# Performance work log

Hardware: AMD Instinct MI355X
Metric: run time of the kernel (lower is better)

The kernel has to match this reference:

```python
import jax, jax.numpy as jnp
import numpy as np

DIM = 512; DEPTH = 2; HEADS = 8; DIM_HEAD = 64; INNER = HEADS * DIM_HEAD
MEM = 16; TOPK = 8; FF = 4 * DIM
NUM_BUCKETS = 32; MAX_DIST = 128
EPS = 1e-5


def _layernorm(x, g, b):
    m = jnp.mean(x, axis=-1, keepdims=True)
    v = jnp.var(x, axis=-1, keepdims=True)
    return (x - m) * jax.lax.rsqrt(v + EPS) * g + b


def _rel_bucket(rel_pos):
    # T5 relative-position bucketing, causal=True (as hardcoded in Encoder)
    num_buckets = NUM_BUCKETS // 2  # 16
    n = -rel_pos
    ret = (n < 0).astype(jnp.int32) * num_buckets
    n = jnp.abs(n)
    max_exact = num_buckets // 2  # 8
    is_small = n < max_exact
    nf = jnp.maximum(n, 1).astype(jnp.float32)  # safe log; masked by is_small where n==0
    val_if_large = max_exact + (
        jnp.log(nf / max_exact) / np.log(MAX_DIST / max_exact) * (num_buckets - max_exact)
    ).astype(jnp.int32)
    val_if_large = jnp.minimum(val_if_large, num_buckets - 1)
    return ret + jnp.where(is_small, n, val_if_large)


def setup_inputs() -> dict:
    key = jax.random.key(0)
    ks = jax.random.split(key, 16)
    B, N = 2, 2048
    w = lambda k, shape, s=0.02: jax.random.normal(k, shape, jnp.float32) * s
    return {
        "x": jax.random.normal(ks[0], (B, N, DIM), jnp.float32),
        "ln1_g": jnp.ones((DEPTH, DIM), jnp.float32),
        "ln1_b": jnp.zeros((DEPTH, DIM), jnp.float32),
        "Wq": w(ks[1], (DEPTH, DIM, INNER)),
        "Wkv": w(ks[2], (DEPTH, DIM, 2 * INNER)),
        "Wo": w(ks[3], (DEPTH, INNER, DIM)),
        "bo": jnp.zeros((DEPTH, DIM), jnp.float32),
        "pre_proj": w(ks[4], (DEPTH, HEADS, HEADS), 1.0),  # torch.randn init
        "mem_k": w(ks[5], (DEPTH, HEADS, MEM, DIM_HEAD), 1.0),
        "mem_v": w(ks[6], (DEPTH, HEADS, MEM, DIM_HEAD), 1.0),
        "ln2_g": jnp.ones((DEPTH, DIM), jnp.float32),
        "ln2_b": jnp.zeros((DEPTH, DIM), jnp.float32),
        "W1": w(ks[7], (DEPTH, DIM, FF)),
        "b1": jnp.zeros((DEPTH, FF), jnp.float32),
        "W2": w(ks[8], (DEPTH, FF, DIM)),
        "b2": jnp.zeros((DEPTH, DIM), jnp.float32),
        "rel_emb": w(ks[9], (NUM_BUCKETS, HEADS)),
    }


def reference(x, ln1_g, ln1_b, Wq, Wkv, Wo, bo, pre_proj, mem_k, mem_v,
              ln2_g, ln2_b, W1, b1, W2, b2, rel_emb):
    B, N, _ = x.shape
    J = N + MEM  # keys include num_mem_kv memory slots
    scale = DIM_HEAD ** -0.5
    # relative position bias, shape (1, H, N, J); same for every layer
    rel = jnp.arange(J)[None, :] - jnp.arange(N)[:, None]
    bias = jnp.transpose(rel_emb[_rel_bucket(rel)], (2, 0, 1))[None]

    for l in range(DEPTH):
        # --- PreNorm(Attention) + residual ---
        h = _layernorm(x, ln1_g[l], ln1_b[l])
        q = (h @ Wq[l]).reshape(B, N, HEADS, DIM_HEAD).transpose(0, 2, 1, 3)
        k, v = jnp.split(h @ Wkv[l], 2, axis=-1)
        k = k.reshape(B, N, HEADS, DIM_HEAD).transpose(0, 2, 1, 3)
        v = v.reshape(B, N, HEADS, DIM_HEAD).transpose(0, 2, 1, 3)
        k = jnp.concatenate([jnp.broadcast_to(mem_k[l], (B, HEADS, MEM, DIM_HEAD)), k], axis=2)
        v = jnp.concatenate([jnp.broadcast_to(mem_v[l], (B, HEADS, MEM, DIM_HEAD)), v], axis=2)
        dots = jnp.einsum('bhid,bhjd->bhij', q, k) * scale
        dots = jnp.einsum('bhij,hk->bkij', dots, pre_proj[l])  # talking heads (pre-softmax)
        dots = dots + bias
        # sparse top-k masking: keep only values >= k-th largest per row
        thr = jax.lax.top_k(dots, TOPK)[0][..., -1:]
        dots = jnp.where(dots < thr, -jnp.inf, dots)
        attn = jax.nn.softmax(dots, axis=-1)
        out = jnp.einsum('bhij,bhjd->bhid', attn, v)
        out = out.transpose(0, 2, 1, 3).reshape(B, N, INNER)
        x = out @ Wo[l] + bo[l] + x
        # --- PreNorm(FeedForward) + residual ---
        h2 = _layernorm(x, ln2_g[l], ln2_b[l])
        x = jax.nn.gelu(h2 @ W1[l] + b1[l], approximate=False) @ W2[l] + b2[l] + x
    return x
```

## Files before the change

### kernel.cpp

```cpp
#include <hip/hip_runtime.h>
#include <cmath>

typedef __bf16 bf16;
typedef __attribute__((ext_vector_type(8))) __bf16 bf16x8;
typedef __attribute__((ext_vector_type(4))) __bf16 bf16x4;
typedef __attribute__((ext_vector_type(4))) float f32x4;

#define NB 2
#define NSEQ 2048
#define NDIM 512
#define NHEADS 8
#define DHEAD 64
#define NMEM 16
#define NJ 2064
#define NJP 2176
#define NFF 2048
#define NROWS (NB*NSEQ)

enum { EPI_QKV = 0, EPI_GELUSPLIT = 1, EPI_RESID = 2 };

template<int BM, int BN, int WAVES_M, int WAVES_N, int EPI>
__global__ __launch_bounds__(256)
void gemm_split(const bf16* __restrict__ A, const bf16* __restrict__ B,
                void* __restrict__ Cv, const float* __restrict__ bias,
                void* __restrict__ Cv2,
                int K, int lda, int ldb, int ldc, int loA, int loB)
{
  constexpr int BK = 32;
  constexpr int WM = BM / WAVES_M;
  constexpr int WN = BN / WAVES_N;
  constexpr int MF = WM / 16;
  constexpr int NF = WN / 16;
  constexpr int AI = (BM * BK * 2) / 4096;
  constexpr int BI = (BN * BK * 2) / 4096;
  __shared__ bf16 Ash[2][BM * BK];
  __shared__ bf16 Asl[2][BM * BK];
  __shared__ bf16 Bsh[2][BN * BK];
  __shared__ bf16 Bsl[2][BN * BK];

  const int bm0 = blockIdx.x * BM;
  const int bn0 = blockIdx.y * BN;
  const int t = threadIdx.x;
  const int wave = t >> 6, lane = t & 63;
  const int wr = wave / WAVES_N, wc = wave % WAVES_N;
  const int sr = t >> 2, sc = t & 3;
  const int frow = lane & 15, fk = (lane >> 4) * 8;

  auto stage = [&](int buf, int k0) {
#pragma unroll
    for (int qi = 0; qi < AI; ++qi) {
      const long long ro = (long long)(bm0 + qi * 64 + sr) * lda + (k0 + sc * 8);
      __builtin_amdgcn_global_load_lds(
          (const __attribute__((address_space(1))) void*)(A + ro),
          (__attribute__((address_space(3))) void*)(&Ash[buf][qi * 2048 + wave * 512]), 16, 0, 0);
      __builtin_amdgcn_global_load_lds(
          (const __attribute__((address_space(1))) void*)(A + ro + loA),
          (__attribute__((address_space(3))) void*)(&Asl[buf][qi * 2048 + wave * 512]), 16, 0, 0);
    }
#pragma unroll
    for (int qi = 0; qi < BI; ++qi) {
      const long long ro = (long long)(bn0 + qi * 64 + sr) * ldb + (k0 + sc * 8);
      __builtin_amdgcn_global_load_lds(
          (const __attribute__((address_space(1))) void*)(B + ro),
          (__attribute__((address_space(3))) void*)(&Bsh[buf][qi * 2048 + wave * 512]), 16, 0, 0);
      __builtin_amdgcn_global_load_lds(
          (const __attribute__((address_space(1))) void*)(B + ro + loB),
          (__attribute__((address_space(3))) void*)(&Bsl[buf][qi * 2048 + wave * 512]), 16, 0, 0);
    }
  };

  f32x4 acc[MF][NF] = {};

  stage(0, 0);
  __syncthreads();
  int cur = 0;
  for (int k0 = 0; k0 < K; k0 += BK) {
    if (k0 + BK < K) stage(cur ^ 1, k0 + BK);
    bf16x8 afh[MF], afl[MF], bfh[NF], bfl[NF];
#pragma unroll
    for (int m = 0; m < MF; m++) {
      afh[m] = *(const bf16x8*)(&Ash[cur][(wr * WM + m * 16 + frow) * BK + fk]);
      afl[m] = *(const bf16x8*)(&Asl[cur][(wr * WM + m * 16 + frow) * BK + fk]);
    }
#pragma unroll
    for (int n = 0; n < NF; n++) {
      bfh[n] = *(const bf16x8*)(&Bsh[cur][(wc * WN + n * 16 + frow) * BK + fk]);
      bfl[n] = *(const bf16x8*)(&Bsl[cur][(wc * WN + n * 16 + frow) * BK + fk]);
    }
#pragma unroll
    for (int m = 0; m < MF; m++)
#pragma unroll
      for (int n = 0; n < NF; n++) {
        acc[m][n] = __builtin_amdgcn_mfma_f32_16x16x32_bf16(afh[m], bfh[n], acc[m][n], 0, 0, 0);
        acc[m][n] = __builtin_amdgcn_mfma_f32_16x16x32_bf16(afl[m], bfh[n], acc[m][n], 0, 0, 0);
        acc[m][n] = __builtin_amdgcn_mfma_f32_16x16x32_bf16(afh[m], bfl[n], acc[m][n], 0, 0, 0);
      }
    __syncthreads();
    cur ^= 1;
  }

#pragma unroll
  for (int m = 0; m < MF; m++) {
#pragma unroll
    for (int n = 0; n < NF; n++) {
      const int row0 = bm0 + wr * WM + m * 16 + (lane >> 4) * 4;
      const int col = bn0 + wc * WN + n * 16 + (lane & 15);
#pragma unroll
      for (int r = 0; r < 4; r++) {
        const float v = acc[m][n][r];
        const long long i = row0 + r;
        if (EPI == EPI_QKV) {
          if (col < NDIM) {
            const float vq = v * 0.125f;
            bf16* base = (bf16*)Cv;
            const long long ih = i * (long long)(2 * NDIM) + col;
            bf16 h = (bf16)vq;
            base[ih] = h;
            base[ih + NDIM] = (bf16)(vq - (float)h);
          } else {
            ((float*)Cv2)[i * (long long)(2 * NDIM) + (col - NDIM)] = v;
          }
        } else if (EPI == EPI_GELUSPLIT) {
          float u = v + bias[col];
          float gl = 0.5f * u * (1.0f + erff(u * 0.7071067811865476f));
          const long long ih = i * (long long)(2 * ldc) + col;
          bf16 h = (bf16)gl;
          ((bf16*)Cv)[ih] = h;
          ((bf16*)Cv)[ih + ldc] = (bf16)(gl - (float)h);
        } else {
          float* xp = ((float*)Cv) + i * ldc + col;
          *xp = *xp + v + bias[col];
        }
      }
    }
  }
}

__global__ __launch_bounds__(256)
void s_gemm_direct(const bf16* __restrict__ Qs, const bf16* __restrict__ Ks,
                   float* __restrict__ S)
{
  const int h = blockIdx.z;
  const int bm0 = blockIdx.x * 128;
  const int bn0 = blockIdx.y * 128;
  const int t = threadIdx.x;
  const int wave = t >> 6, lane = t & 63;
  const int wr = wave >> 1, wc = wave & 1;
  const int frow = lane & 15, fk = (lane >> 4) * 8;

  bf16x8 ah[4][2], al[4][2];
#pragma unroll
  for (int m = 0; m < 4; m++)
#pragma unroll
    for (int kk = 0; kk < 2; kk++) {
      const bf16* ap = Qs + (long long)(bm0 + wr * 64 + m * 16 + frow) * 1024
                     + h * 64 + kk * 32 + fk;
      ah[m][kk] = *(const bf16x8*)(ap);
      al[m][kk] = *(const bf16x8*)(ap + 512);
    }

  f32x4 acc[4][4] = {};
#pragma unroll
  for (int n = 0; n < 4; n++) {
    bf16x8 bh[2], bl[2];
#pragma unroll
    for (int kk = 0; kk < 2; kk++) {
      const bf16* bp = Ks + (long long)(bn0 + wc * 64 + n * 16 + frow) * 1024
                     + h * 64 + kk * 32 + fk;
      bh[kk] = *(const bf16x8*)(bp);
      bl[kk] = *(const bf16x8*)(bp + 512);
    }
#pragma unroll
    for (int m = 0; m < 4; m++)
#pragma unroll
      for (int kk = 0; kk < 2; kk++) {
        acc[m][n] = __builtin_amdgcn_mfma_f32_16x16x32_bf16(ah[m][kk], bh[kk], acc[m][n], 0, 0, 0);
        acc[m][n] = __builtin_amdgcn_mfma_f32_16x16x32_bf16(al[m][kk], bh[kk], acc[m][n], 0, 0, 0);
        acc[m][n] = __builtin_amdgcn_mfma_f32_16x16x32_bf16(ah[m][kk], bl[kk], acc[m][n], 0, 0, 0);
      }
  }

#pragma unroll
  for (int m = 0; m < 4; m++) {
#pragma unroll
    for (int n = 0; n < 4; n++) {
      const int row0 = bm0 + wr * 64 + m * 16 + (lane >> 4) * 4;
      const int col = bn0 + wc * 64 + n * 16 + (lane & 15);
#pragma unroll
      for (int r = 0; r < 4; r++)
        S[(long long)(row0 + r) * (NHEADS * NJP) + h * NJP + col] = acc[m][n][r];
    }
  }
}

__global__ __launch_bounds__(256)
void ln_kernel(const float* __restrict__ x, const float* __restrict__ g,
               const float* __restrict__ b, bf16* __restrict__ out)
{
  const int row = blockIdx.x * 4 + (threadIdx.x >> 6);
  const int lane = threadIdx.x & 63;
  const float* xr = x + (long long)row * NDIM;
  float4 a0 = ((const float4*)xr)[lane];
  float4 a1 = ((const float4*)xr)[lane + 64];
  float s = a0.x + a0.y + a0.z + a0.w + a1.x + a1.y + a1.z + a1.w;
  float ss = a0.x * a0.x + a0.y * a0.y + a0.z * a0.z + a0.w * a0.w
           + a1.x * a1.x + a1.y * a1.y + a1.z * a1.z + a1.w * a1.w;
#pragma unroll
  for (int d = 1; d < 64; d <<= 1) {
    s += __shfl_xor(s, d, 64);
    ss += __shfl_xor(ss, d, 64);
  }
  const float mean = s * (1.0f / NDIM);
  const float var = ss * (1.0f / NDIM) - mean * mean;
  const float rs = rsqrtf(var + 1e-5f);
  float4 g0 = ((const float4*)g)[lane], g1 = ((const float4*)g)[lane + 64];
  float4 b0 = ((const float4*)b)[lane], b1 = ((const float4*)b)[lane + 64];
  bf16* orow = out + (long long)row * (2 * NDIM);
  float y[8] = {
    (a0.x - mean) * rs * g0.x + b0.x, (a0.y - mean) * rs * g0.y + b0.y,
    (a0.z - mean) * rs * g0.z + b0.z, (a0.w - mean) * rs * g0.w + b0.w,
    (a1.x - mean) * rs * g1.x + b1.x, (a1.y - mean) * rs * g1.y + b1.y,
    (a1.z - mean) * rs * g1.z + b1.z, (a1.w - mean) * rs * g1.w + b1.w };
  bf16x4 h0, h1, l0, l1;
#pragma unroll
  for (int j = 0; j < 4; j++) {
    bf16 h = (bf16)y[j];      h0[j] = h;  l0[j] = (bf16)(y[j] - (float)h);
    bf16 h2 = (bf16)y[4 + j]; h1[j] = h2; l1[j] = (bf16)(y[4 + j] - (float)h2);
  }
  *(bf16x4*)(orow + lane * 4) = h0;
  *(bf16x4*)(orow + 256 + lane * 4) = h1;
  *(bf16x4*)(orow + 512 + lane * 4) = l0;
  *(bf16x4*)(orow + 768 + lane * 4) = l1;
}

__global__ __launch_bounds__(256)
void build_ks(const float* __restrict__ kv, const float* __restrict__ mem_k_l,
              bf16* __restrict__ Ks)
{
  const long long idx = (long long)blockIdx.x * 256 + threadIdx.x;
  const int c = (int)(idx & 511);
  const int j = (int)((idx >> 9) % NJP);
  const int bb = (int)(idx / ((long long)NJP * NDIM));
  const int h = c >> 6, d = c & 63;
  float kval;
  if (j < NMEM) kval = mem_k_l[(h * NMEM + j) * DHEAD + d];
  else if (j < NJ) kval = kv[(long long)(bb * NSEQ + (j - NMEM)) * (2 * NDIM) + c];
  else kval = 0.f;
  bf16 hv = (bf16)kval;
  const long long ro = ((long long)bb * NJP + j) * (2 * NDIM) + c;
  Ks[ro] = hv;
  Ks[ro + NDIM] = (bf16)(kval - (float)hv);
}

__global__ __launch_bounds__(512)
void mix_topk_gather(const float* __restrict__ S, const float* __restrict__ kv,
                     const float* __restrict__ mem_v_l, const float* __restrict__ pp,
                     const float* __restrict__ table, bf16* __restrict__ obufs,
                     int b)
{
  __shared__ float sm[4 * NJP];
  const int i = blockIdx.x;
  const int k = threadIdx.x >> 6;
  const int lane = threadIdx.x & 63;
  const float* srow = S + (long long)i * (NHEADS * NJP);

  float pk[8];
#pragma unroll
  for (int h = 0; h < 8; h++) pk[h] = pp[h * 8 + k];

  float v[34];

  {
    const float4* src = (const float4*)srow;
    float4* dst = (float4*)sm;
    for (int t = threadIdx.x; t < NJP; t += 512) dst[t] = src[t];
  }
  __syncthreads();
#pragma unroll
  for (int t = 0; t < 8; t++) {
    const int j0 = 256 * t + 4 * lane;
    const float* tb = table + (j0 - i + 2047) * 8 + k;
    float4 a;
    a.x = tb[0]; a.y = tb[8]; a.z = tb[16]; a.w = tb[24];
#pragma unroll
    for (int h = 0; h < 4; h++) {
      const float4 s4 = *(const float4*)(sm + h * NJP + j0);
      a.x = fmaf(s4.x, pk[h], a.x);
      a.y = fmaf(s4.y, pk[h], a.y);
      a.z = fmaf(s4.z, pk[h], a.z);
      a.w = fmaf(s4.w, pk[h], a.w);
    }
    v[t * 4 + 0] = a.x; v[t * 4 + 1] = a.y; v[t * 4 + 2] = a.z; v[t * 4 + 3] = a.w;
  }
  {
    const int j0 = 2048 + 2 * lane;
    const int jc = j0 < 2062 ? j0 : 2062;
    const float* tb = table + (jc - i + 2047) * 8 + k;
    float ax = tb[0], ay = tb[8];
#pragma unroll
    for (int h = 0; h < 4; h++) {
      const float2 s2 = *(const float2*)(sm + h * NJP + j0);
      ax = fmaf(s2.x, pk[h], ax);
      ay = fmaf(s2.y, pk[h], ay);
    }
    v[32] = ax; v[33] = ay;
  }
  __syncthreads();

  {
    const float4* src = (const float4*)(srow + 4 * NJP);
    float4* dst = (float4*)sm;
    for (int t = threadIdx.x; t < NJP; t += 512) dst[t] = src[t];
  }
  __syncthreads();

  float t8[8];
#pragma unroll
  for (int m = 0; m < 8; m++) t8[m] = -3.0e38f;

#pragma unroll
  for (int t = 0; t < 8; t++) {
    const int j0 = 256 * t + 4 * lane;
    float4 a;
    a.x = v[t * 4 + 0]; a.y = v[t * 4 + 1]; a.z = v[t * 4 + 2]; a.w = v[t * 4 + 3];
#pragma unroll
    for (int h = 4; h < 8; h++) {
      const float4 s4 = *(const float4*)(sm + (h - 4) * NJP + j0);
      a.x = fmaf(s4.x, pk[h], a.x);
      a.y = fmaf(s4.y, pk[h], a.y);
      a.z = fmaf(s4.z, pk[h], a.z);
      a.w = fmaf(s4.w, pk[h], a.w);
    }
    v[t * 4 + 0] = a.x; v[t * 4 + 1] = a.y; v[t * 4 + 2] = a.z; v[t * 4 + 3] = a.w;
#pragma unroll
    for (int e = 0; e < 4; e++) {
      float x = v[t * 4 + e];
#pragma unroll
      for (int m = 0; m < 8; m++) {
        const float hi = fmaxf(t8[m], x);
        x = fminf(t8[m], x);
        t8[m] = hi;
      }
    }
  }
  {
    const int j0 = 2048 + 2 * lane;
    float ax = v[32], ay = v[33];
#pragma unroll
    for (int h = 4; h < 8; h++) {
      const float2 s2 = *(const float2*)(sm + (h - 4) * NJP + j0);
      ax = fmaf(s2.x, pk[h], ax);
      ay = fmaf(s2.y, pk[h], ay);
    }
    v[32] = (j0 < NJ) ? ax : -1e30f;
    v[33] = (j0 + 1 < NJ) ? ay : -1e30f;
#pragma unroll
    for (int e = 32; e < 34; e++) {
      float x = v[e];
#pragma unroll
      for (int m = 0; m < 8; m++) {
        const float hi = fmaxf(t8[m], x);
        x = fminf(t8[m], x);
        t8[m] = hi;
      }
    }
  }

#pragma unroll
  for (int d = 1; d < 64; d <<= 1) {
    float o[8], m8[8];
#pragma unroll
    for (int m = 0; m < 8; m++) o[m] = __shfl_xor(t8[m], d, 64);
#pragma unroll
    for (int m = 0; m < 8; m++) m8[m] = fmaxf(t8[m], o[7 - m]);
#define CX(a, bq) { float hi = fmaxf(m8[a], m8[bq]); float lo = fminf(m8[a], m8[bq]); m8[a] = hi; m8[bq] = lo; }
    CX(0, 4) CX(1, 5) CX(2, 6) CX(3, 7)
    CX(0, 2) CX(1, 3) CX(4, 6) CX(5, 7)
    CX(0, 1) CX(2, 3) CX(4, 5) CX(6, 7)
#undef CX
#pragma unroll
    for (int m = 0; m < 8; m++) t8[m] = m8[m];
  }
  const float mx = t8[0];
  const float thr = t8[7];
  float denom = 0.f;
#pragma unroll
  for (int m = 0; m < 8; m++) denom += expf(t8[m] - mx);
  const float inv = 1.0f / denom;

  float acc = 0.f;
#pragma unroll
  for (int t = 0; t < 8; t++) {
#pragma unroll
    for (int e = 0; e < 4; e++) {
      unsigned long long mball = __ballot(v[t * 4 + e] >= thr);
      while (mball) {
        const int l = __builtin_ctzll(mball);
        mball &= mball - 1;
        const int jj = 256 * t + 4 * l + e;
        const float sv = __shfl(v[t * 4 + e], l);
        const float w = expf(sv - mx) * inv;
        const float vv = (jj < NMEM)
            ? mem_v_l[(k * NMEM + jj) * DHEAD + lane]
            : kv[(long long)(b * NSEQ + (jj - NMEM)) * (2 * NDIM) + NDIM + k * DHEAD + lane];
        acc = fmaf(w, vv, acc);
      }
    }
  }
#pragma unroll
  for (int e = 0; e < 2; e++) {
    unsigned long long mball = __ballot(v[32 + e] >= thr);
    while (mball) {
      const int l = __builtin_ctzll(mball);
      mball &= mball - 1;
      const int jj = 2048 + 2 * l + e;
      const float sv = __shfl(v[32 + e], l);
      const float w = expf(sv - mx) * inv;
      const float vv = (jj < NMEM)
          ? mem_v_l[(k * NMEM + jj) * DHEAD + lane]
          : kv[(long long)(b * NSEQ + (jj - NMEM)) * (2 * NDIM) + NDIM + k * DHEAD + lane];
      acc = fmaf(w, vv, acc);
    }
  }

  const long long orow = (long long)(b * NSEQ + i) * (2 * NDIM) + k * DHEAD + lane;
  bf16 h = (bf16)acc;
  obufs[orow] = h;
  obufs[orow + NDIM] = (bf16)(acc - (float)h);
}

__global__ __launch_bounds__(256)
void transpose_split(const float* __restrict__ in, bf16* __restrict__ out,
                     int R, int C)
{
  const long long idx = (long long)blockIdx.x * 256 + threadIdx.x;
  if (idx >= (long long)R * C) return;
  const int r = (int)(idx / C);
  const int c = (int)(idx % C);
  float v = in[idx];
  bf16 h = (bf16)v;
  out[(long long)c * (2 * R) + r] = h;
  out[(long long)c * (2 * R) + R + r] = (bf16)(v - (float)h);
}

__global__ __launch_bounds__(256)
void build_bias(const float* __restrict__ rel_emb, float* __restrict__ table)
{
  const int idx = blockIdx.x * 256 + threadIdx.x;
  if (idx >= 4111 * 8) return;
  const int h = idx & 7;
  const int rel = (idx >> 3) - 2047;
  const int n = -rel;
  const int ret = (n < 0) ? 16 : 0;
  const int na = n < 0 ? -n : n;
  int bucket;
  if (na < 8) {
    bucket = ret + na;
  } else {
    int vl = 8 + (int)(log2((double)na * 0.125) * 2.0);
    vl = vl < 15 ? vl : 15;
    bucket = ret + vl;
  }
  table[idx] = rel_emb[bucket * 8 + h];
}

extern "C" void kernel_launch(void* const* d_in, const int* in_sizes, int n_in,
                              void* d_out, int out_size, void* d_ws, size_t ws_size,
                              hipStream_t stream)
{
  const float* x_in    = (const float*)d_in[0];
  const float* ln1_g   = (const float*)d_in[1];
  const float* ln1_b   = (const float*)d_in[2];
  const float* Wq      = (const float*)d_in[3];
  const float* Wkv     = (const float*)d_in[4];
  const float* Wo      = (const float*)d_in[5];
  const float* bo      = (const float*)d_in[6];
  const float* pre_proj= (const float*)d_in[7];
  const float* mem_k   = (const float*)d_in[8];
  const float* mem_v   = (const float*)d_in[9];
  const float* ln2_g   = (const float*)d_in[10];
  const float* ln2_b   = (const float*)d_in[11];
  const float* W1      = (const float*)d_in[12];
  const float* b1      = (const float*)d_in[13];
  const float* W2      = (const float*)d_in[14];
  const float* b2      = (const float*)d_in[15];
  const float* rel_emb = (const float*)d_in[16];

  char* p = (char*)d_ws;
  auto alloc = [&](size_t bytes) -> char* {
    char* r = p;
    p += (bytes + 255) & ~(size_t)255;
    return r;
  };

  float* x    = (float*)alloc((size_t)NROWS * NDIM * 4);
  char*  RA   = alloc((size_t)NROWS * 2 * NDIM * 2);
  bf16*  hs    = (bf16*)RA;
  bf16*  obufs = (bf16*)RA;
  char*  RB   = alloc((size_t)NROWS * 2 * NFF * 2);
  bf16*  Qs    = (bf16*)RB;
  bf16*  Ks    = (bf16*)(RB + (size_t)NROWS * 2 * NDIM * 2);
  bf16*  tbufs = (bf16*)RB;
  float* kv   = (float*)alloc((size_t)NROWS * 2 * NDIM * 4);
  float* S    = (float*)alloc((size_t)NSEQ * NHEADS * NJP * 4);
  bf16*  WqkvT= (bf16*)alloc((size_t)2 * 3 * NDIM * 2 * NDIM * 2);
  bf16*  WoT  = (bf16*)alloc((size_t)2 * NDIM * 2 * NDIM * 2);
  bf16*  W1T  = (bf16*)alloc((size_t)2 * NFF * 2 * NDIM * 2);
  bf16*  W2T  = (bf16*)alloc((size_t)2 * NDIM * 2 * NFF * 2);
  float* table= (float*)alloc((size_t)4111 * 8 * 4);

  hipMemcpyAsync(x, x_in, (size_t)NROWS * NDIM * 4, hipMemcpyDeviceToDevice, stream);
  build_bias<<<(4111 * 8 + 255) / 256, 256, 0, stream>>>(rel_emb, table);
  for (int l = 0; l < 2; l++) {
    bf16* WqkvT_l = WqkvT + (size_t)l * 3 * NDIM * 2 * NDIM;
    transpose_split<<<(NDIM * NDIM + 255) / 256, 256, 0, stream>>>(
        Wq + (size_t)l * NDIM * NDIM, WqkvT_l, NDIM, NDIM);
    transpose_split<<<(2 * NDIM * NDIM + 255) / 256, 256, 0, stream>>>(
        Wkv + (size_t)l * NDIM * 2 * NDIM, WqkvT_l + (size_t)NDIM * 2 * NDIM,
        NDIM, 2 * NDIM);
    transpose_split<<<(NDIM * NDIM + 255) / 256, 256, 0, stream>>>(
        Wo + (size_t)l * NDIM * NDIM, WoT + (size_t)l * NDIM * 2 * NDIM, NDIM, NDIM);
    transpose_split<<<(NDIM * NFF + 255) / 256, 256, 0, stream>>>(
        W1 + (size_t)l * NDIM * NFF, W1T + (size_t)l * NFF * 2 * NDIM, NDIM, NFF);
    transpose_split<<<(NFF * NDIM + 255) / 256, 256, 0, stream>>>(
        W2 + (size_t)l * NFF * NDIM, W2T + (size_t)l * NDIM * 2 * NFF, NFF, NDIM);
  }

  for (int l = 0; l < 2; l++) {
    const bf16* WqkvT_l = WqkvT + (size_t)l * 3 * NDIM * 2 * NDIM;
    const bf16* WoT_l  = WoT + (size_t)l * NDIM * 2 * NDIM;
    const bf16* W1T_l  = W1T + (size_t)l * NFF * 2 * NDIM;
    const bf16* W2T_l  = W2T + (size_t)l * NDIM * 2 * NFF;
    const float* mem_v_l = mem_v + (size_t)l * NHEADS * NMEM * DHEAD;

    ln_kernel<<<NROWS / 4, 256, 0, stream>>>(x, ln1_g + l * NDIM, ln1_b + l * NDIM, hs);
    gemm_split<128, 128, 2, 2, EPI_QKV><<<dim3(NROWS / 128, 12), 256, 0, stream>>>(
        hs, WqkvT_l, Qs, nullptr, kv, NDIM, 2 * NDIM, 2 * NDIM, 0, NDIM, NDIM);
    build_ks<<<(int)(((long long)NB * NJP * NDIM) / 256), 256, 0, stream>>>(
        kv, mem_k + (size_t)l * NHEADS * NMEM * DHEAD, Ks);

    for (int b = 0; b < NB; b++) {
      s_gemm_direct<<<dim3(NSEQ / 128, NJP / 128, NHEADS), 256, 0, stream>>>(
          Qs + (long long)b * NSEQ * 1024, Ks + (long long)b * NJP * 1024, S);
      mix_topk_gather<<<NSEQ, 512, 0, stream>>>(
          S, kv, mem_v_l, pre_proj + l * 64, table, obufs, b);
    }

    gemm_split<128, 64, 2, 2, EPI_RESID><<<dim3(NROWS / 128, NDIM / 64), 256, 0, stream>>>(
        obufs, WoT_l, x, bo + l * NDIM, nullptr, NDIM, 2 * NDIM, 2 * NDIM, NDIM, NDIM, NDIM);

    ln_kernel<<<NROWS / 4, 256, 0, stream>>>(x, ln2_g + l * NDIM, ln2_b + l * NDIM, hs);
    gemm_split<128, 128, 2, 2, EPI_GELUSPLIT><<<dim3(NROWS / 128, NFF / 128), 256, 0, stream>>>(
        hs, W1T_l, tbufs, b1 + l * NFF, nullptr, NDIM, 2 * NDIM, 2 * NDIM, NFF, NDIM, NDIM);
    gemm_split<128, 64, 2, 2, EPI_RESID><<<dim3(NROWS / 128, NDIM / 64), 256, 0, stream>>>(
        tbufs, W2T_l, x, b2 + l * NDIM, nullptr, NFF, 2 * NFF, 2 * NFF, NDIM, NFF, NFF);
  }

  hipMemcpyAsync(d_out, x, (size_t)out_size * 4, hipMemcpyDeviceToDevice, stream);
}
```

Before: 947.1 us.

## Fuse K split into QKV epilogue, transpose bias table, stream S directly in topk

The QKV GEMM epilogue now writes K straight into the split bf16 Ks buffer, and only the mem/padding rows are filled by a small edge kernel. This removes the full build_ks pass and the fp32 K round trip. The bias table is re-laid out per head so contiguous loads replace strided ones. The mix/topk kernel now reads S rows directly from global memory instead of staging them through shared memory with barriers, and uses fast __expf. The risks are less-coalesced scattered epilogue stores and slightly lower exp precision.

```diff
diff --git a/kernel.cpp b/kernel.cpp
--- a/kernel.cpp
+++ b/kernel.cpp
@@ -16,6 +16,7 @@
 #define NJP 2176
 #define NFF 2048
 #define NROWS (NB*NSEQ)
+#define TBL 4111
 
 enum { EPI_QKV = 0, EPI_GELUSPLIT = 1, EPI_RESID = 2 };
 
@@ -23,7 +24,7 @@
 __global__ __launch_bounds__(256)
 void gemm_split(const bf16* __restrict__ A, const bf16* __restrict__ B,
                 void* __restrict__ Cv, const float* __restrict__ bias,
-                void* __restrict__ Cv2,
+                void* __restrict__ Cv2, void* __restrict__ Cv3,
                 int K, int lda, int ldb, int ldc, int loA, int loB)
 {
   constexpr int BK = 32;
@@ -110,6 +111,8 @@
         const float v = acc[m][n][r];
         const long long i = row0 + r;
         if (EPI == EPI_QKV) {
+          const int bb = (int)(i >> 11);
+          const int il = (int)(i & 2047);
           if (col < NDIM) {
             const float vq = v * 0.125f;
             bf16* base = (bf16*)Cv;
@@ -117,8 +120,15 @@
             bf16 h = (bf16)vq;
             base[ih] = h;
             base[ih + NDIM] = (bf16)(vq - (float)h);
+          } else if (col < 2 * NDIM) {
+            bf16* ks = (bf16*)Cv3;
+            const long long ih = ((long long)bb * NJP + il + NMEM) * (long long)(2 * NDIM)
+                               + (col - NDIM);
+            bf16 h = (bf16)v;
+            ks[ih] = h;
+            ks[ih + NDIM] = (bf16)(v - (float)h);
           } else {
-            ((float*)Cv2)[i * (long long)(2 * NDIM) + (col - NDIM)] = v;
+            ((float*)Cv2)[i * (long long)NDIM + (col - 2 * NDIM)] = v;
           }
         } else if (EPI == EPI_GELUSPLIT) {
           float u = v + bias[col];
@@ -234,18 +244,15 @@
 }
 
 __global__ __launch_bounds__(256)
-void build_ks(const float* __restrict__ kv, const float* __restrict__ mem_k_l,
-              bf16* __restrict__ Ks)
-{
-  const long long idx = (long long)blockIdx.x * 256 + threadIdx.x;
-  const int c = (int)(idx & 511);
-  const int j = (int)((idx >> 9) % NJP);
-  const int bb = (int)(idx / ((long long)NJP * NDIM));
-  const int h = c >> 6, d = c & 63;
-  float kval;
-  if (j < NMEM) kval = mem_k_l[(h * NMEM + j) * DHEAD + d];
-  else if (j < NJ) kval = kv[(long long)(bb * NSEQ + (j - NMEM)) * (2 * NDIM) + c];
-  else kval = 0.f;
+void ks_edges(const float* __restrict__ mem_k_l, bf16* __restrict__ Ks)
+{
+  const int idx = blockIdx.x * 256 + threadIdx.x;
+  const int c = idx & 511;
+  const int jj = (idx >> 9) & 127;
+  const int bb = idx >> 16;
+  const int j = (jj < NMEM) ? jj : (jj - NMEM + NJ);
+  float kval = 0.f;
+  if (jj < NMEM) kval = mem_k_l[((c >> 6) * NMEM + jj) * DHEAD + (c & 63)];
   bf16 hv = (bf16)kval;
   const long long ro = ((long long)bb * NJP + j) * (2 * NDIM) + c;
   Ks[ro] = hv;
@@ -253,12 +260,11 @@
 }
 
 __global__ __launch_bounds__(512)
-void mix_topk_gather(const float* __restrict__ S, const float* __restrict__ kv,
+void mix_topk_gather(const float* __restrict__ S, const float* __restrict__ kvV,
                      const float* __restrict__ mem_v_l, const float* __restrict__ pp,
-                     const float* __restrict__ table, bf16* __restrict__ obufs,
+                     const float* __restrict__ table2, bf16* __restrict__ obufs,
                      int b)
 {
-  __shared__ float sm[4 * NJP];
   const int i = blockIdx.x;
   const int k = threadIdx.x >> 6;
   const int lane = threadIdx.x & 63;
@@ -267,102 +273,57 @@
   float pk[8];
 #pragma unroll
   for (int h = 0; h < 8; h++) pk[h] = pp[h * 8 + k];
+  const float* t2k = table2 + k * TBL + (2047 - i);
 
   float v[34];
-
-  {
-    const float4* src = (const float4*)srow;
-    float4* dst = (float4*)sm;
-    for (int t = threadIdx.x; t < NJP; t += 512) dst[t] = src[t];
-  }
-  __syncthreads();
 #pragma unroll
   for (int t = 0; t < 8; t++) {
     const int j0 = 256 * t + 4 * lane;
-    const float* tb = table + (j0 - i + 2047) * 8 + k;
-    float4 a;
-    a.x = tb[0]; a.y = tb[8]; a.z = tb[16]; a.w = tb[24];
-#pragma unroll
-    for (int h = 0; h < 4; h++) {
-      const float4 s4 = *(const float4*)(sm + h * NJP + j0);
-      a.x = fmaf(s4.x, pk[h], a.x);
-      a.y = fmaf(s4.y, pk[h], a.y);
-      a.z = fmaf(s4.z, pk[h], a.z);
-      a.w = fmaf(s4.w, pk[h], a.w);
-    }
-    v[t * 4 + 0] = a.x; v[t * 4 + 1] = a.y; v[t * 4 + 2] = a.z; v[t * 4 + 3] = a.w;
+    v[4 * t + 0] = t2k[j0];
+    v[4 * t + 1] = t2k[j0 + 1];
+    v[4 * t + 2] = t2k[j0 + 2];
+    v[4 * t + 3] = t2k[j0 + 3];
   }
   {
     const int j0 = 2048 + 2 * lane;
     const int jc = j0 < 2062 ? j0 : 2062;
-    const float* tb = table + (jc - i + 2047) * 8 + k;
-    float ax = tb[0], ay = tb[8];
-#pragma unroll
-    for (int h = 0; h < 4; h++) {
-      const float2 s2 = *(const float2*)(sm + h * NJP + j0);
-      ax = fmaf(s2.x, pk[h], ax);
-      ay = fmaf(s2.y, pk[h], ay);
-    }
-    v[32] = ax; v[33] = ay;
-  }
-  __syncthreads();
-
-  {
-    const float4* src = (const float4*)(srow + 4 * NJP);
-    float4* dst = (float4*)sm;
-    for (int t = threadIdx.x; t < NJP; t += 512) dst[t] = src[t];
-  }
-  __syncthreads();
-
-  float t8[8];
-#pragma unroll
-  for (int m = 0; m < 8; m++) t8[m] = -3.0e38f;
-
-#pragma unroll
-  for (int t = 0; t < 8; t++) {
-    const int j0 = 256 * t + 4 * lane;
-    float4 a;
-    a.x = v[t * 4 + 0]; a.y = v[t * 4 + 1]; a.z = v[t * 4 + 2]; a.w = v[t * 4 + 3];
-#pragma unroll
-    for (int h = 4; h < 8; h++) {
-      const float4 s4 = *(const float4*)(sm + (h - 4) * NJP + j0);
-      a.x = fmaf(s4.x, pk[h], a.x);
-      a.y = fmaf(s4.y, pk[h], a.y);
-      a.z = fmaf(s4.z, pk[h], a.z);
-      a.w = fmaf(s4.w, pk[h], a.w);
-    }
-    v[t * 4 + 0] = a.x; v[t * 4 + 1] = a.y; v[t * 4 + 2] = a.z; v[t * 4 + 3] = a.w;
-#pragma unroll
-    for (int e = 0; e < 4; e++) {
-      float x = v[t * 4 + e];
-#pragma unroll
-      for (int m = 0; m < 8; m++) {
-        const float hi = fmaxf(t8[m], x);
-        x = fminf(t8[m], x);
-        t8[m] = hi;
-      }
-    }
+    v[32] = t2k[jc];
+    v[33] = t2k[jc + 1];
+  }
+
+#pragma unroll
+  for (int h = 0; h < 8; h++) {
+    const float* sp = srow + h * NJP;
+    const float w = pk[h];
+#pragma unroll
+    for (int t = 0; t < 8; t++) {
+      const float4 s4 = *(const float4*)(sp + 256 * t + 4 * lane);
+      v[4 * t + 0] = fmaf(s4.x, w, v[4 * t + 0]);
+      v[4 * t + 1] = fmaf(s4.y, w, v[4 * t + 1]);
+      v[4 * t + 2] = fmaf(s4.z, w, v[4 * t + 2]);
+      v[4 * t + 3] = fmaf(s4.w, w, v[4 * t + 3]);
+    }
+    const float2 s2 = *(const float2*)(sp + 2048 + 2 * lane);
+    v[32] = fmaf(s2.x, w, v[32]);
+    v[33] = fmaf(s2.y, w, v[33]);
   }
   {
     const int j0 = 2048 + 2 * lane;
-    float ax = v[32], ay = v[33];
-#pragma unroll
-    for (int h = 4; h < 8; h++) {
-      const float2 s2 = *(const float2*)(sm + (h - 4) * NJP + j0);
-      ax = fmaf(s2.x, pk[h], ax);
-      ay = fmaf(s2.y, pk[h], ay);
-    }
-    v[32] = (j0 < NJ) ? ax : -1e30f;
-    v[33] = (j0 + 1 < NJ) ? ay : -1e30f;
-#pragma unroll
-    for (int e = 32; e < 34; e++) {
-      float x = v[e];
-#pragma unroll
-      for (int m = 0; m < 8; m++) {
-        const float hi = fmaxf(t8[m], x);
-        x = fminf(t8[m], x);
-        t8[m] = hi;
-      }
+    if (j0 >= NJ) v[32] = -1e30f;
+    if (j0 + 1 >= NJ) v[33] = -1e30f;
+  }
+
+  float t8[8];
+#pragma unroll
+  for (int m = 0; m < 8; m++) t8[m] = -3.0e38f;
+#pragma unroll
+  for (int e = 0; e < 34; e++) {
+    float x = v[e];
+#pragma unroll
+    for (int m = 0; m < 8; m++) {
+      const float hi = fmaxf(t8[m], x);
+      x = fminf(t8[m], x);
+      t8[m] = hi;
     }
   }
 
@@ -385,7 +346,7 @@
   const float thr = t8[7];
   float denom = 0.f;
 #pragma unroll
-  for (int m = 0; m < 8; m++) denom += expf(t8[m] - mx);
+  for (int m = 0; m < 8; m++) denom += __expf(t8[m] - mx);
   const float inv = 1.0f / denom;
 
   float acc = 0.f;
@@ -399,10 +360,10 @@
         mball &= mball - 1;
         const int jj = 256 * t + 4 * l + e;
         const float sv = __shfl(v[t * 4 + e], l);
-        const float w = expf(sv - mx) * inv;
+        const float w = __expf(sv - mx) * inv;
         const float vv = (jj < NMEM)
             ? mem_v_l[(k * NMEM + jj) * DHEAD + lane]
-            : kv[(long long)(b * NSEQ + (jj - NMEM)) * (2 * NDIM) + NDIM + k * DHEAD + lane];
+            : kvV[(long long)(b * NSEQ + (jj - NMEM)) * NDIM + k * DHEAD + lane];
         acc = fmaf(w, vv, acc);
       }
     }
@@ -415,10 +376,10 @@
       mball &= mball - 1;
       const int jj = 2048 + 2 * l + e;
       const float sv = __shfl(v[32 + e], l);
-      const float w = expf(sv - mx) * inv;
+      const float w = __expf(sv - mx) * inv;
       const float vv = (jj < NMEM)
           ? mem_v_l[(k * NMEM + jj) * DHEAD + lane]
-          : kv[(long long)(b * NSEQ + (jj - NMEM)) * (2 * NDIM) + NDIM + k * DHEAD + lane];
+          : kvV[(long long)(b * NSEQ + (jj - NMEM)) * NDIM + k * DHEAD + lane];
       acc = fmaf(w, vv, acc);
     }
   }
@@ -444,12 +405,12 @@
 }
 
 __global__ __launch_bounds__(256)
-void build_bias(const float* __restrict__ rel_emb, float* __restrict__ table)
+void build_bias2(const float* __restrict__ rel_emb, float* __restrict__ table2)
 {
   const int idx = blockIdx.x * 256 + threadIdx.x;
-  if (idx >= 4111 * 8) return;
-  const int h = idx & 7;
-  const int rel = (idx >> 3) - 2047;
+  if (idx >= 8 * TBL) return;
+  const int k = idx / TBL;
+  const int rel = (idx % TBL) - 2047;
   const int n = -rel;
   const int ret = (n < 0) ? 16 : 0;
   const int na = n < 0 ? -n : n;
@@ -461,7 +422,7 @@
     vl = vl < 15 ? vl : 15;
     bucket = ret + vl;
   }
-  table[idx] = rel_emb[bucket * 8 + h];
+  table2[idx] = rel_emb[bucket * 8 + k];
 }
 
 extern "C" void kernel_launch(void* const* d_in, const int* in_sizes, int n_in,
@@ -501,16 +462,16 @@
   bf16*  Qs    = (bf16*)RB;
   bf16*  Ks    = (bf16*)(RB + (size_t)NROWS * 2 * NDIM * 2);
   bf16*  tbufs = (bf16*)RB;
-  float* kv   = (float*)alloc((size_t)NROWS * 2 * NDIM * 4);
+  float* kvV  = (float*)alloc((size_t)NROWS * NDIM * 4);
   float* S    = (float*)alloc((size_t)NSEQ * NHEADS * NJP * 4);
   bf16*  WqkvT= (bf16*)alloc((size_t)2 * 3 * NDIM * 2 * NDIM * 2);
   bf16*  WoT  = (bf16*)alloc((size_t)2 * NDIM * 2 * NDIM * 2);
   bf16*  W1T  = (bf16*)alloc((size_t)2 * NFF * 2 * NDIM * 2);
   bf16*  W2T  = (bf16*)alloc((size_t)2 * NDIM * 2 * NFF * 2);
-  float* table= (float*)alloc((size_t)4111 * 8 * 4);
+  float* table2= (float*)alloc((size_t)8 * TBL * 4);
 
   hipMemcpyAsync(x, x_in, (size_t)NROWS * NDIM * 4, hipMemcpyDeviceToDevice, stream);
-  build_bias<<<(4111 * 8 + 255) / 256, 256, 0, stream>>>(rel_emb, table);
+  build_bias2<<<(8 * TBL + 255) / 256, 256, 0, stream>>>(rel_emb, table2);
   for (int l = 0; l < 2; l++) {
     bf16* WqkvT_l = WqkvT + (size_t)l * 3 * NDIM * 2 * NDIM;
     transpose_split<<<(NDIM * NDIM + 255) / 256, 256, 0, stream>>>(
@@ -535,25 +496,28 @@
 
     ln_kernel<<<NROWS / 4, 256, 0, stream>>>(x, ln1_g + l * NDIM, ln1_b + l * NDIM, hs);
     gemm_split<128, 128, 2, 2, EPI_QKV><<<dim3(NROWS / 128, 12), 256, 0, stream>>>(
-        hs, WqkvT_l, Qs, nullptr, kv, NDIM, 2 * NDIM, 2 * NDIM, 0, NDIM, NDIM);
-    build_ks<<<(int)(((long long)NB * NJP * NDIM) / 256), 256, 0, stream>>>(
-        kv, mem_k + (size_t)l * NHEADS * NMEM * DHEAD, Ks);
+        hs, WqkvT_l, Qs, nullptr, kvV, Ks, NDIM, 2 * NDIM, 2 * NDIM, 0, NDIM, NDIM);
+    ks_edges<<<(2 * 128 * 512) / 256, 256, 0, stream>>>(
+        mem_k + (size_t)l * NHEADS * NMEM * DHEAD, Ks);
 
     for (int b = 0; b < NB; b++) {
       s_gemm_direct<<<dim3(NSEQ / 128, NJP / 128, NHEADS), 256, 0, stream>>>(
           Qs + (long long)b * NSEQ * 1024, Ks + (long long)b * NJP * 1024, S);
       mix_topk_gather<<<NSEQ, 512, 0, stream>>>(
-          S, kv, mem_v_l, pre_proj + l * 64, table, obufs, b);
+          S, kvV, mem_v_l, pre_proj + l * 64, table2, obufs, b);
     }
 
     gemm_split<128, 64, 2, 2, EPI_RESID><<<dim3(NROWS / 128, NDIM / 64), 256, 0, stream>>>(
-        obufs, WoT_l, x, bo + l * NDIM, nullptr, NDIM, 2 * NDIM, 2 * NDIM, NDIM, NDIM, NDIM);
+        obufs, WoT_l, x, bo + l * NDIM, nullptr, nullptr,
+        NDIM, 2 * NDIM, 2 * NDIM, NDIM, NDIM, NDIM);
 
     ln_kernel<<<NROWS / 4, 256, 0, stream>>>(x, ln2_g + l * NDIM, ln2_b + l * NDIM, hs);
     gemm_split<128, 128, 2, 2, EPI_GELUSPLIT><<<dim3(NROWS / 128, NFF / 128), 256, 0, stream>>>(
-        hs, W1T_l, tbufs, b1 + l * NFF, nullptr, NDIM, 2 * NDIM, 2 * NDIM, NFF, NDIM, NDIM);
+        hs, W1T_l, tbufs, b1 + l * NFF, nullptr, nullptr,
+        NDIM, 2 * NDIM, 2 * NDIM, NFF, NDIM, NDIM);
     gemm_split<128, 64, 2, 2, EPI_RESID><<<dim3(NROWS / 128, NDIM / 64), 256, 0, stream>>>(
-        tbufs, W2T_l, x, b2 + l * NDIM, nullptr, NFF, 2 * NFF, 2 * NFF, NDIM, NFF, NFF);
+        tbufs, W2T_l, x, b2 + l * NDIM, nullptr, nullptr,
+        NFF, 2 * NFF, 2 * NFF, NDIM, NFF, NFF);
   }
 
   hipMemcpyAsync(d_out, x, (size_t)out_size * 4, hipMemcpyDeviceToDevice, stream);
```

New measurement: 881.7 us. -6.9%, faster.
